# Kernel optimization log

Measured on AMD Instinct MI355X. Metric: run time of the kernel, lower is better.

The kernel has to match this reference:

```python
import jax, jax.numpy as jnp
import numpy as np
import math

HIDDEN = 1024
HEADS = 16
HEAD_DIM = HIDDEN // HEADS
B, S = 2, 2048


def _xavier(key, shape):
    fan_in, fan_out = shape[1], shape[0]
    limit = math.sqrt(6.0 / (fan_in + fan_out))
    return jax.random.uniform(key, shape, jnp.float32, -limit, limit)


def setup_inputs() -> dict:
    key = jax.random.key(0)
    ks = jax.random.split(key, 5)
    x = jax.random.normal(ks[0], (B, S, HIDDEN), jnp.float32)
    # torch Linear stores weight as [out, in]; y = x @ W.T + b
    Wq = _xavier(ks[1], (HIDDEN, HIDDEN))
    Wk = _xavier(ks[2], (HIDDEN, HIDDEN))
    Wv = _xavier(ks[3], (HIDDEN, HIDDEN))
    Wo = _xavier(ks[4], (HIDDEN, HIDDEN))
    bq = jnp.zeros((HIDDEN,), jnp.float32)
    bk = jnp.zeros((HIDDEN,), jnp.float32)
    bv = jnp.zeros((HIDDEN,), jnp.float32)
    bo = jnp.zeros((HIDDEN,), jnp.float32)
    return {"x": x, "Wq": Wq, "bq": bq, "Wk": Wk, "bk": bk,
            "Wv": Wv, "bv": bv, "Wo": Wo, "bo": bo}


def reference(x, Wq, bq, Wk, bk, Wv, bv, Wo, bo):
    b, s, d = x.shape
    h, hd = HEADS, HEAD_DIM
    q = (x @ Wq.T + bq).reshape(b, s, h, hd).transpose(0, 2, 1, 3)  # [b,h,s,hd]
    k = (x @ Wk.T + bk).reshape(b, s, h, hd).transpose(0, 2, 1, 3)
    v = (x @ Wv.T + bv).reshape(b, s, h, hd).transpose(0, 2, 1, 3)
    scores = jnp.einsum('bhqd,bhkd->bhqk', q, k) / math.sqrt(hd)
    causal = jnp.tril(jnp.ones((s, s), bool))
    scores = jnp.where(causal, scores, -jnp.inf)
    attn = jax.nn.softmax(scores, axis=-1)
    out = jnp.einsum('bhqk,bhkd->bhqd', attn, v)  # [b,h,s,hd]
    out = out.transpose(0, 2, 1, 3).reshape(b, s, d)
    return out @ Wo.T + bo
```

## Files before the change

### kernel.cpp

```cpp
#include <hip/hip_runtime.h>
#include <hip/hip_bf16.h>


typedef __hip_bfloat16 bf16;
typedef __attribute__((ext_vector_type(8))) short short8;
typedef __attribute__((ext_vector_type(4))) short short4v;
typedef __attribute__((ext_vector_type(4))) float f32x4;

#define MFMA16(a, b, c) __builtin_amdgcn_mfma_f32_16x16x32_bf16((a), (b), (c), 0, 0, 0)

__device__ __forceinline__ void load_lds16(const void* g, void* l) {
  __builtin_amdgcn_global_load_lds(
      (const __attribute__((address_space(1))) void*)g,
      (__attribute__((address_space(3))) void*)l, 16, 0, 0);
}

#define QSCALE 0.18033688f

__global__ __launch_bounds__(256) void cvt_kernel(
    const float* __restrict__ x, const float* __restrict__ wq,
    const float* __restrict__ wk, const float* __restrict__ wv,
    const float* __restrict__ wo, bf16* __restrict__ xb,
    bf16* __restrict__ wcat) {
  const int bx = blockIdx.x;
  const float* src;
  bf16* dst;
  int ib;
  if (bx < 4096) { src = x; dst = xb; ib = bx; }
  else {
    const int wseg = (bx - 4096) >> 10;
    ib = (bx - 4096) & 1023;
    src = wseg == 0 ? wq : wseg == 1 ? wk : wseg == 2 ? wv : wo;
    dst = wcat + (size_t)wseg * 1048576;
  }
  const int i = (ib * 256 + threadIdx.x) * 4;
  const float4 v = *(const float4*)(src + i);
  short4v p;
  *(__hip_bfloat162*)&p = __float22bfloat162_rn(float2{v.x, v.y});
  *((__hip_bfloat162*)&p + 1) = __float22bfloat162_rn(float2{v.z, v.w});
  *(short4v*)(dst + i) = p;
}

__global__ __launch_bounds__(256) void qkv_kernel(
    const bf16* __restrict__ x, const bf16* __restrict__ Wcat,
    const float* __restrict__ bq, const float* __restrict__ bk,
    const float* __restrict__ bv, bf16* __restrict__ Qb,
    bf16* __restrict__ Kb, bf16* __restrict__ Vtg) {
  constexpr int K = 1024;
  __shared__ bf16 As[128 * 64];
  __shared__ bf16 Bs[128 * 64];
  const int t = threadIdx.x;
  const int lane = t & 63, w = t >> 6;
  const int quad = lane >> 4, r = lane & 15;
  const int m0 = blockIdx.y * 128;
  const int ncol = blockIdx.x * 128;
  const int seg = ncol >> 10;
  const int n0 = ncol & 1023;
  const int wm = w >> 1, wn = w & 1;

  f32x4 acc[4][4] = {};

  for (int k0 = 0; k0 < K; k0 += 64) {
    __syncthreads();
#pragma unroll
    for (int p = 0; p < 4; ++p) {
      const int c = p * 256 + w * 64 + lane;
      const int row = c >> 3;
      const int scb = (c & 7) ^ (row & 7);
      load_lds16(x + (size_t)(m0 + row) * K + k0 + scb * 8, As + c * 8);
    }
#pragma unroll
    for (int p = 0; p < 4; ++p) {
      const int c = p * 256 + w * 64 + lane;
      const int row = c >> 3;
      const int scb = (c & 7) ^ (row & 7);
      load_lds16(Wcat + (size_t)(ncol + row) * K + k0 + scb * 8, Bs + c * 8);
    }
    __syncthreads();
    short8 af[4][2], bfr[4][2];
#pragma unroll
    for (int ks = 0; ks < 2; ++ks) {
#pragma unroll
      for (int i = 0; i < 4; ++i) {
        const int ra = wm * 64 + i * 16 + r;
        af[i][ks] = *(const short8*)(As + ra * 64 +
                                     (((ks * 4 + quad) ^ (ra & 7)) * 8));
        const int rb = wn * 64 + i * 16 + r;
        bfr[i][ks] = *(const short8*)(Bs + rb * 64 +
                                      (((ks * 4 + quad) ^ (rb & 7)) * 8));
      }
    }
#pragma unroll
    for (int ks = 0; ks < 2; ++ks)
#pragma unroll
      for (int i = 0; i < 4; ++i)
#pragma unroll
        for (int j = 0; j < 4; ++j)
          acc[i][j] = MFMA16(af[i][ks], bfr[j][ks], acc[i][j]);
  }

  const float* bias = seg == 0 ? bq : seg == 1 ? bk : bv;
  const float scale = seg == 0 ? QSCALE : 1.0f;
  bf16* dst01 = seg == 0 ? Qb : Kb;
#pragma unroll
  for (int i = 0; i < 4; ++i) {
    const int m = m0 + wm * 64 + i * 16 + quad * 4;
#pragma unroll
    for (int j = 0; j < 4; ++j) {
      const int nn = n0 + wn * 64 + j * 16 + r;
      const float bv_ = bias[nn];
      if (seg == 2) {
        short4v pk;
        *(__hip_bfloat162*)&pk = __float22bfloat162_rn(
            float2{acc[i][j][0] + bv_, acc[i][j][1] + bv_});
        *((__hip_bfloat162*)&pk + 1) = __float22bfloat162_rn(
            float2{acc[i][j][2] + bv_, acc[i][j][3] + bv_});
        *(short4v*)(Vtg + (size_t)nn * 4096 + m) = pk;
      } else {
#pragma unroll
        for (int g = 0; g < 4; ++g)
          dst01[(size_t)(m + g) * 1024 + nn] =
              __float2bfloat16((acc[i][j][g] + bv_) * scale);
      }
    }
  }
}

__global__ __launch_bounds__(256) void proj_kernel(const bf16* __restrict__ X,
                                                   const bf16* __restrict__ W,
                                                   const float* __restrict__ bias,
                                                   float* __restrict__ Y) {
  constexpr int K = 1024, N = 1024;
  __shared__ bf16 As[64 * 64];
  __shared__ bf16 Bs[128 * 64];
  const int t = threadIdx.x;
  const int lane = t & 63, w = t >> 6;
  const int quad = lane >> 4, r = lane & 15;
  const int m0 = blockIdx.y * 64, n0 = blockIdx.x * 128;
  const int wm = w >> 1, wn = w & 1;

  f32x4 acc[2][4] = {};

  for (int k0 = 0; k0 < K; k0 += 64) {
    __syncthreads();
#pragma unroll
    for (int p = 0; p < 2; ++p) {
      const int c = p * 256 + w * 64 + lane;
      const int row = c >> 3;
      const int scb = (c & 7) ^ (row & 7);
      load_lds16(X + (size_t)(m0 + row) * K + k0 + scb * 8, As + c * 8);
    }
#pragma unroll
    for (int p = 0; p < 4; ++p) {
      const int c = p * 256 + w * 64 + lane;
      const int row = c >> 3;
      const int scb = (c & 7) ^ (row & 7);
      load_lds16(W + (size_t)(n0 + row) * K + k0 + scb * 8, Bs + c * 8);
    }
    __syncthreads();
    short8 af[2][2], bfr[4][2];
#pragma unroll
    for (int ks = 0; ks < 2; ++ks) {
#pragma unroll
      for (int i = 0; i < 2; ++i) {
        const int ra = wm * 32 + i * 16 + r;
        af[i][ks] = *(const short8*)(As + ra * 64 +
                                     (((ks * 4 + quad) ^ (ra & 7)) * 8));
      }
#pragma unroll
      for (int j = 0; j < 4; ++j) {
        const int rb = wn * 64 + j * 16 + r;
        bfr[j][ks] = *(const short8*)(Bs + rb * 64 +
                                      (((ks * 4 + quad) ^ (rb & 7)) * 8));
      }
    }
#pragma unroll
    for (int ks = 0; ks < 2; ++ks)
#pragma unroll
      for (int i = 0; i < 2; ++i)
#pragma unroll
        for (int j = 0; j < 4; ++j)
          acc[i][j] = MFMA16(af[i][ks], bfr[j][ks], acc[i][j]);
  }
#pragma unroll
  for (int i = 0; i < 2; ++i) {
    const int m = m0 + wm * 32 + i * 16 + quad * 4;
#pragma unroll
    for (int j = 0; j < 4; ++j) {
      const int n = n0 + wn * 64 + j * 16 + r;
      const float bv = bias[n];
#pragma unroll
      for (int g = 0; g < 4; ++g)
        Y[(size_t)(m + g) * N + n] = acc[i][j][g] + bv;
    }
  }
}

__global__ __launch_bounds__(256) void attn_kernel(const bf16* __restrict__ Qb,
                                                   const bf16* __restrict__ Kb,
                                                   const bf16* __restrict__ Vtg,
                                                   bf16* __restrict__ Ob) {
  const int pair = blockIdx.x, h = blockIdx.y, b = blockIdx.z;
  const int t = threadIdx.x;
  const int lane = t & 63, w = t >> 6;
  const int quad = lane >> 4, r = lane & 15;

  __shared__ bf16 Ks[128 * 64];
  __shared__ bf16 Vt[64 * 128];
  __shared__ bf16 Pl[4][2][16 * 128];

  const bf16 *kp[4], *vp[4];
  bf16 *klds[4], *vlds[4];
#pragma unroll
  for (int p = 0; p < 4; ++p) {
    const int c = p * 256 + w * 64 + lane;
    const int rowK = c >> 3, scbK = (c & 7) ^ (rowK & 7);
    const int rowV = c >> 4, scbV = (c & 15) ^ (rowV & 15);
    klds[p] = Ks + c * 8;
    vlds[p] = Vt + c * 8;
    kp[p] = Kb + (size_t)(b * 2048 + rowK) * 1024 + h * 64 + scbK * 8;
    vp[p] = Vtg + (size_t)(h * 64 + rowV) * 4096 + b * 2048 + scbV * 8;
  }

  const int jlo = pair, jhi = 31 - pair;
  const int nkt_lo = jlo / 2 + 1, nkt_hi = jhi / 2 + 1;
  const int qrow_lo = jlo * 64 + w * 16 + r;
  const int qrow_hi = jhi * 64 + w * 16 + r;

  short8 qfl[2], qfh[2];
#pragma unroll
  for (int ks = 0; ks < 2; ++ks) {
    qfl[ks] = *(const short8*)(Qb + (size_t)(b * 2048 + qrow_lo) * 1024 +
                               h * 64 + ks * 32 + quad * 8);
    qfh[ks] = *(const short8*)(Qb + (size_t)(b * 2048 + qrow_hi) * 1024 +
                               h * 64 + ks * 32 + quad * 8);
  }

  f32x4 oh[4] = {}, ol[4] = {};
  float lsh = 0.f, lsl = 0.f;

  for (int kt = 0; kt < nkt_hi; ++kt) {
    const int k0 = kt * 128;
    __syncthreads();
#pragma unroll
    for (int p = 0; p < 4; ++p) load_lds16(kp[p], klds[p]);
#pragma unroll
    for (int p = 0; p < 4; ++p) load_lds16(vp[p], vlds[p]);
#pragma unroll
    for (int p = 0; p < 4; ++p) { kp[p] += 128 * 1024; vp[p] += 128; }
    __syncthreads();

    const bool lo_act = (kt < nkt_lo);

    auto s_phase = [&](const short8* qf, int qrow, bool mask, int qi,
                       float& lsum) {
      f32x4 st[8] = {};
#pragma unroll
      for (int ks = 0; ks < 2; ++ks) {
        short8 kf[8];
#pragma unroll
        for (int mt = 0; mt < 8; ++mt) {
          const int key = mt * 16 + r;
          kf[mt] = *(const short8*)(Ks + key * 64 +
                                    (((ks * 4 + quad) ^ (key & 7)) * 8));
        }
#pragma unroll
        for (int mt = 0; mt < 8; ++mt) st[mt] = MFMA16(kf[mt], qf[ks], st[mt]);
      }
      if (mask) {
#pragma unroll
        for (int mt = 0; mt < 8; ++mt)
#pragma unroll
          for (int g = 0; g < 4; ++g) {
            const int key = k0 + mt * 16 + quad * 4 + g;
            if (key > qrow) st[mt][g] = -1e30f;
          }
      }
#pragma unroll
      for (int mt = 0; mt < 8; ++mt) {
        const float p0 = exp2f(st[mt][0]), p1 = exp2f(st[mt][1]);
        const float p2 = exp2f(st[mt][2]), p3 = exp2f(st[mt][3]);
        lsum += (p0 + p1) + (p2 + p3);
        short4v pk;
        *(__hip_bfloat162*)&pk = __float22bfloat162_rn(float2{p0, p1});
        *((__hip_bfloat162*)&pk + 1) = __float22bfloat162_rn(float2{p2, p3});
        const int key8 = mt * 2 + (quad >> 1);
        const int off = r * 128 + ((key8 ^ (r & 15)) * 8) + (quad & 1) * 4;
        *(short4v*)(&Pl[w][qi][off]) = pk;
      }
    };

    s_phase(qfh, qrow_hi, kt == nkt_hi - 1, 0, lsh);
    if (lo_act) s_phase(qfl, qrow_lo, kt == nkt_lo - 1, 1, lsl);

    asm volatile("s_waitcnt lgkmcnt(0)" ::: "memory");

#pragma unroll
    for (int ks = 0; ks < 4; ++ks) {
      short8 vf[4];
#pragma unroll
      for (int mt = 0; mt < 4; ++mt) {
        const int d = mt * 16 + r;
        vf[mt] = *(const short8*)(Vt + d * 128 +
                                  (((ks * 4 + quad) ^ (d & 15)) * 8));
      }
      const int poff = r * 128 + (((ks * 4 + quad) ^ (r & 15)) * 8);
      const short8 pfh = *(const short8*)(Pl[w][0] + poff);
#pragma unroll
      for (int mt = 0; mt < 4; ++mt) oh[mt] = MFMA16(vf[mt], pfh, oh[mt]);
      if (lo_act) {
        const short8 pfl = *(const short8*)(Pl[w][1] + poff);
#pragma unroll
        for (int mt = 0; mt < 4; ++mt) ol[mt] = MFMA16(vf[mt], pfl, ol[mt]);
      }
    }
  }

  lsh += __shfl_xor(lsh, 16);
  lsh += __shfl_xor(lsh, 32);
  lsl += __shfl_xor(lsl, 16);
  lsl += __shfl_xor(lsl, 32);
  const float invh = 1.f / lsh, invl = 1.f / lsl;

#pragma unroll
  for (int mt = 0; mt < 4; ++mt) {
    const int d0 = mt * 16 + quad * 4;
    short4v ph, pl2;
    *(__hip_bfloat162*)&ph = __float22bfloat162_rn(
        float2{oh[mt][0] * invh, oh[mt][1] * invh});
    *((__hip_bfloat162*)&ph + 1) = __float22bfloat162_rn(
        float2{oh[mt][2] * invh, oh[mt][3] * invh});
    *(short4v*)(Ob + (size_t)(b * 2048 + qrow_hi) * 1024 + h * 64 + d0) = ph;
    *(__hip_bfloat162*)&pl2 = __float22bfloat162_rn(
        float2{ol[mt][0] * invl, ol[mt][1] * invl});
    *((__hip_bfloat162*)&pl2 + 1) = __float22bfloat162_rn(
        float2{ol[mt][2] * invl, ol[mt][3] * invl});
    *(short4v*)(Ob + (size_t)(b * 2048 + qrow_lo) * 1024 + h * 64 + d0) = pl2;
  }
}

extern "C" void kernel_launch(void* const* d_in, const int* in_sizes, int n_in,
                              void* d_out, int out_size, void* d_ws, size_t ws_size,
                              hipStream_t stream) {
  const float* x  = (const float*)d_in[0];
  const float* Wq = (const float*)d_in[1];
  const float* bq = (const float*)d_in[2];
  const float* Wk = (const float*)d_in[3];
  const float* bk = (const float*)d_in[4];
  const float* Wv = (const float*)d_in[5];
  const float* bv = (const float*)d_in[6];
  const float* Wo = (const float*)d_in[7];
  const float* bo = (const float*)d_in[8];
  float* out = (float*)d_out;

  bf16* xb   = (bf16*)d_ws;
  bf16* wcat = xb + (size_t)4096 * 1024;
  bf16* wob  = wcat + (size_t)3 * 1024 * 1024;
  bf16* Qb   = wcat + (size_t)4 * 1024 * 1024;
  bf16* Kb   = Qb  + (size_t)4096 * 1024;
  bf16* Vtg  = Kb  + (size_t)4096 * 1024;
  bf16* Ob   = Vtg + (size_t)4096 * 1024;
  const size_t need = ((size_t)4096 * 1024 * 5 + (size_t)1024 * 1024 * 4) * 2;
  if (ws_size < need) return;

  cvt_kernel<<<8192, 256, 0, stream>>>(x, Wq, Wk, Wv, Wo, xb, wcat);
  qkv_kernel<<<dim3(24, 32), 256, 0, stream>>>(xb, wcat, bq, bk, bv,
                                               Qb, Kb, Vtg);
  attn_kernel<<<dim3(16, 16, 2), 256, 0, stream>>>(Qb, Kb, Vtg, Ob);
  proj_kernel<<<dim3(8, 64), 256, 0, stream>>>(Ob, wob, bo, out);
}
```

Measured before the change: 184.6 us.

## Split each key tile across two wave groups in attention and reduce via LDS

Doubles the attention block to 512 threads: each group of four waves processes half of every 128-key tile for the same query rows. Partial outputs and row sums are merged through LDS at the end before normalization. This raises the number of waves per CU to better hide latency in the causal attention loop. It costs extra barriers and an LDS reduction at the end, and doubles the number of threads sharing each tile load.

```diff
diff --git a/kernel.cpp b/kernel.cpp
--- a/kernel.cpp
+++ b/kernel.cpp
@@ -196,24 +196,24 @@
   }
 }
 
-__global__ __launch_bounds__(256) void attn_kernel(const bf16* __restrict__ Qb,
-                                                   const bf16* __restrict__ Kb,
-                                                   const bf16* __restrict__ Vtg,
-                                                   bf16* __restrict__ Ob) {
+__global__ __launch_bounds__(512, 4) void attn_kernel(
+    const bf16* __restrict__ Qb, const bf16* __restrict__ Kb,
+    const bf16* __restrict__ Vtg, bf16* __restrict__ Ob) {
   const int pair = blockIdx.x, h = blockIdx.y, b = blockIdx.z;
   const int t = threadIdx.x;
   const int lane = t & 63, w = t >> 6;
+  const int qsub = w & 3, kh = w >> 2;
   const int quad = lane >> 4, r = lane & 15;
 
   __shared__ bf16 Ks[128 * 64];
   __shared__ bf16 Vt[64 * 128];
-  __shared__ bf16 Pl[4][2][16 * 128];
-
-  const bf16 *kp[4], *vp[4];
-  bf16 *klds[4], *vlds[4];
-#pragma unroll
-  for (int p = 0; p < 4; ++p) {
-    const int c = p * 256 + w * 64 + lane;
+  __shared__ bf16 Pl[8][2][16 * 64];
+
+  const bf16 *kp[2], *vp[2];
+  bf16 *klds[2], *vlds[2];
+#pragma unroll
+  for (int p = 0; p < 2; ++p) {
+    const int c = p * 512 + w * 64 + lane;
     const int rowK = c >> 3, scbK = (c & 7) ^ (rowK & 7);
     const int rowV = c >> 4, scbV = (c & 15) ^ (rowV & 15);
     klds[p] = Ks + c * 8;
@@ -224,8 +224,8 @@
 
   const int jlo = pair, jhi = 31 - pair;
   const int nkt_lo = jlo / 2 + 1, nkt_hi = jhi / 2 + 1;
-  const int qrow_lo = jlo * 64 + w * 16 + r;
-  const int qrow_hi = jhi * 64 + w * 16 + r;
+  const int qrow_lo = jlo * 64 + qsub * 16 + r;
+  const int qrow_hi = jhi * 64 + qsub * 16 + r;
 
   short8 qfl[2], qfh[2];
 #pragma unroll
@@ -243,41 +243,41 @@
     const int k0 = kt * 128;
     __syncthreads();
 #pragma unroll
-    for (int p = 0; p < 4; ++p) load_lds16(kp[p], klds[p]);
-#pragma unroll
-    for (int p = 0; p < 4; ++p) load_lds16(vp[p], vlds[p]);
-#pragma unroll
-    for (int p = 0; p < 4; ++p) { kp[p] += 128 * 1024; vp[p] += 128; }
+    for (int p = 0; p < 2; ++p) load_lds16(kp[p], klds[p]);
+#pragma unroll
+    for (int p = 0; p < 2; ++p) load_lds16(vp[p], vlds[p]);
+#pragma unroll
+    for (int p = 0; p < 2; ++p) { kp[p] += 128 * 1024; vp[p] += 128; }
     __syncthreads();
 
     const bool lo_act = (kt < nkt_lo);
 
     auto s_phase = [&](const short8* qf, int qrow, bool mask, int qi,
                        float& lsum) {
-      f32x4 st[8] = {};
+      f32x4 st[4] = {};
 #pragma unroll
       for (int ks = 0; ks < 2; ++ks) {
-        short8 kf[8];
-#pragma unroll
-        for (int mt = 0; mt < 8; ++mt) {
-          const int key = mt * 16 + r;
+        short8 kf[4];
+#pragma unroll
+        for (int mt = 0; mt < 4; ++mt) {
+          const int key = kh * 64 + mt * 16 + r;
           kf[mt] = *(const short8*)(Ks + key * 64 +
-                                    (((ks * 4 + quad) ^ (key & 7)) * 8));
+                                    (((ks * 4 + quad) ^ (r & 7)) * 8));
         }
 #pragma unroll
-        for (int mt = 0; mt < 8; ++mt) st[mt] = MFMA16(kf[mt], qf[ks], st[mt]);
+        for (int mt = 0; mt < 4; ++mt) st[mt] = MFMA16(kf[mt], qf[ks], st[mt]);
       }
       if (mask) {
 #pragma unroll
-        for (int mt = 0; mt < 8; ++mt)
+        for (int mt = 0; mt < 4; ++mt)
 #pragma unroll
           for (int g = 0; g < 4; ++g) {
-            const int key = k0 + mt * 16 + quad * 4 + g;
+            const int key = k0 + kh * 64 + mt * 16 + quad * 4 + g;
             if (key > qrow) st[mt][g] = -1e30f;
           }
       }
 #pragma unroll
-      for (int mt = 0; mt < 8; ++mt) {
+      for (int mt = 0; mt < 4; ++mt) {
         const float p0 = exp2f(st[mt][0]), p1 = exp2f(st[mt][1]);
         const float p2 = exp2f(st[mt][2]), p3 = exp2f(st[mt][3]);
         lsum += (p0 + p1) + (p2 + p3);
@@ -285,7 +285,7 @@
         *(__hip_bfloat162*)&pk = __float22bfloat162_rn(float2{p0, p1});
         *((__hip_bfloat162*)&pk + 1) = __float22bfloat162_rn(float2{p2, p3});
         const int key8 = mt * 2 + (quad >> 1);
-        const int off = r * 128 + ((key8 ^ (r & 15)) * 8) + (quad & 1) * 4;
+        const int off = r * 64 + ((key8 ^ (r & 7)) * 8) + (quad & 1) * 4;
         *(short4v*)(&Pl[w][qi][off]) = pk;
       }
     };
@@ -296,15 +296,15 @@
     asm volatile("s_waitcnt lgkmcnt(0)" ::: "memory");
 
 #pragma unroll
-    for (int ks = 0; ks < 4; ++ks) {
+    for (int ks = 0; ks < 2; ++ks) {
       short8 vf[4];
 #pragma unroll
       for (int mt = 0; mt < 4; ++mt) {
         const int d = mt * 16 + r;
         vf[mt] = *(const short8*)(Vt + d * 128 +
-                                  (((ks * 4 + quad) ^ (d & 15)) * 8));
-      }
-      const int poff = r * 128 + (((ks * 4 + quad) ^ (r & 15)) * 8);
+                                  (((kh * 8 + ks * 4 + quad) ^ r) * 8));
+      }
+      const int poff = r * 64 + (((ks * 4 + quad) ^ (r & 7)) * 8);
       const short8 pfh = *(const short8*)(Pl[w][0] + poff);
 #pragma unroll
       for (int mt = 0; mt < 4; ++mt) oh[mt] = MFMA16(vf[mt], pfh, oh[mt]);
@@ -316,26 +316,61 @@
     }
   }
 
-  lsh += __shfl_xor(lsh, 16);
-  lsh += __shfl_xor(lsh, 32);
-  lsl += __shfl_xor(lsl, 16);
-  lsl += __shfl_xor(lsl, 32);
-  const float invh = 1.f / lsh, invl = 1.f / lsl;
-
-#pragma unroll
-  for (int mt = 0; mt < 4; ++mt) {
-    const int d0 = mt * 16 + quad * 4;
-    short4v ph, pl2;
-    *(__hip_bfloat162*)&ph = __float22bfloat162_rn(
-        float2{oh[mt][0] * invh, oh[mt][1] * invh});
-    *((__hip_bfloat162*)&ph + 1) = __float22bfloat162_rn(
-        float2{oh[mt][2] * invh, oh[mt][3] * invh});
-    *(short4v*)(Ob + (size_t)(b * 2048 + qrow_hi) * 1024 + h * 64 + d0) = ph;
-    *(__hip_bfloat162*)&pl2 = __float22bfloat162_rn(
-        float2{ol[mt][0] * invl, ol[mt][1] * invl});
-    *((__hip_bfloat162*)&pl2 + 1) = __float22bfloat162_rn(
-        float2{ol[mt][2] * invl, ol[mt][3] * invl});
-    *(short4v*)(Ob + (size_t)(b * 2048 + qrow_lo) * 1024 + h * 64 + d0) = pl2;
+  float* xch = (float*)&Pl[0][0][0];
+  const int xi = (qsub * 64 + lane) * 20;
+  __syncthreads();
+  if (kh == 1) {
+#pragma unroll
+    for (int mt = 0; mt < 4; ++mt) *(f32x4*)(xch + xi + mt * 4) = oh[mt];
+    xch[xi + 16] = lsh;
+  }
+  __syncthreads();
+  if (kh == 0) {
+#pragma unroll
+    for (int mt = 0; mt < 4; ++mt) {
+      const f32x4 v = *(const f32x4*)(xch + xi + mt * 4);
+#pragma unroll
+      for (int g = 0; g < 4; ++g) oh[mt][g] += v[g];
+    }
+    lsh += xch[xi + 16];
+  }
+  __syncthreads();
+  if (kh == 1) {
+#pragma unroll
+    for (int mt = 0; mt < 4; ++mt) *(f32x4*)(xch + xi + mt * 4) = ol[mt];
+    xch[xi + 16] = lsl;
+  }
+  __syncthreads();
+  if (kh == 0) {
+#pragma unroll
+    for (int mt = 0; mt < 4; ++mt) {
+      const f32x4 v = *(const f32x4*)(xch + xi + mt * 4);
+#pragma unroll
+      for (int g = 0; g < 4; ++g) ol[mt][g] += v[g];
+    }
+    lsl += xch[xi + 16];
+
+    lsh += __shfl_xor(lsh, 16);
+    lsh += __shfl_xor(lsh, 32);
+    lsl += __shfl_xor(lsl, 16);
+    lsl += __shfl_xor(lsl, 32);
+    const float invh = 1.f / lsh, invl = 1.f / lsl;
+
+#pragma unroll
+    for (int mt = 0; mt < 4; ++mt) {
+      const int d0 = mt * 16 + quad * 4;
+      short4v ph, pl2;
+      *(__hip_bfloat162*)&ph = __float22bfloat162_rn(
+          float2{oh[mt][0] * invh, oh[mt][1] * invh});
+      *((__hip_bfloat162*)&ph + 1) = __float22bfloat162_rn(
+          float2{oh[mt][2] * invh, oh[mt][3] * invh});
+      *(short4v*)(Ob + (size_t)(b * 2048 + qrow_hi) * 1024 + h * 64 + d0) = ph;
+      *(__hip_bfloat162*)&pl2 = __float22bfloat162_rn(
+          float2{ol[mt][0] * invl, ol[mt][1] * invl});
+      *((__hip_bfloat162*)&pl2 + 1) = __float22bfloat162_rn(
+          float2{ol[mt][2] * invl, ol[mt][3] * invl});
+      *(short4v*)(Ob + (size_t)(b * 2048 + qrow_lo) * 1024 + h * 64 + d0) = pl2;
+    }
   }
 }
 
@@ -366,6 +401,6 @@
   cvt_kernel<<<8192, 256, 0, stream>>>(x, Wq, Wk, Wv, Wo, xb, wcat);
   qkv_kernel<<<dim3(24, 32), 256, 0, stream>>>(xb, wcat, bq, bk, bv,
                                                Qb, Kb, Vtg);
-  attn_kernel<<<dim3(16, 16, 2), 256, 0, stream>>>(Qb, Kb, Vtg, Ob);
+  attn_kernel<<<dim3(16, 16, 2), 512, 0, stream>>>(Qb, Kb, Vtg, Ob);
   proj_kernel<<<dim3(8, 64), 256, 0, stream>>>(Ob, wob, bo, out);
 }
```

Result: slower. 188.5 us (+2.1%).
